# Kernel optimization log

Hardware: AMD Instinct MI355X
Metric: run time of the kernel (lower is better)

The kernel has to match this reference:

```python
import jax, jax.numpy as jnp
import numpy as np

N = 8192   # number of points
K = 16     # knn_graph k (loop=True -> self included)
C = 256    # conv hidden width
H = 128    # classifier hidden width


def _lin_init(key, fan_in, fan_out):
    s = 1.0 / np.sqrt(fan_in)
    kw, kb = jax.random.split(key)
    W = jax.random.uniform(kw, (fan_in, fan_out), minval=-s, maxval=s, dtype=jnp.float32)
    b = jax.random.uniform(kb, (fan_out,), minval=-s, maxval=s, dtype=jnp.float32)
    return W, b


def setup_inputs() -> dict:
    key = jax.random.key(0)
    ks = jax.random.split(key, 10)
    pos = jax.random.normal(ks[0], (N, 3), dtype=jnp.float32)
    # conv1 local_nn: Linear(3+3,256), ReLU, Linear(256,256)
    c1_W1, c1_b1 = _lin_init(ks[1], 3 + 3, C)
    c1_W2, c1_b2 = _lin_init(ks[2], C, C)
    # conv2/conv3 local_nn: Linear(256+3,256), ReLU, Linear(256,256)
    c2_W1, c2_b1 = _lin_init(ks[3], C + 3, C)
    c2_W2, c2_b2 = _lin_init(ks[4], C, C)
    c3_W1, c3_b1 = _lin_init(ks[5], C + 3, C)
    c3_W2, c3_b2 = _lin_init(ks[6], C, C)
    # classifier: Linear(256,128), ReLU, Linear(128,128), ReLU, Linear(128,1)
    h_W1, h_b1 = _lin_init(ks[7], C, H)
    h_W2, h_b2 = _lin_init(ks[8], H, H)
    h_W3, h_b3 = _lin_init(ks[9], H, 1)
    return dict(pos=pos,
                c1_W1=c1_W1, c1_b1=c1_b1, c1_W2=c1_W2, c1_b2=c1_b2,
                c2_W1=c2_W1, c2_b1=c2_b1, c2_W2=c2_W2, c2_b2=c2_b2,
                c3_W1=c3_W1, c3_b1=c3_b1, c3_W2=c3_W2, c3_b2=c3_b2,
                h_W1=h_W1, h_b1=h_b1, h_W2=h_W2, h_b2=h_b2, h_W3=h_W3, h_b3=h_b3)


def _knn_idx(pos):
    # squared pairwise distances via the gram trick; [N,N]
    sq = jnp.sum(pos * pos, axis=-1)
    d2 = sq[:, None] + sq[None, :] - 2.0 * (pos @ pos.T)
    # k smallest distances (self distance ~0 -> self loop, matching loop=True)
    _, idx = jax.lax.top_k(-d2, K)  # [N,K] neighbor (source) indices per target
    return idx


def _pointnet_conv(h, rel, idx, W1, b1, W2, b2):
    # message = local_nn(concat(x_j, pos_j - pos_i)); aggregate = max over neighbors
    e = jnp.concatenate([h[idx], rel], axis=-1)          # [N,K,Cin+3]
    m = jax.nn.relu(e @ W1 + b1) @ W2 + b2               # [N,K,C]
    return jnp.max(m, axis=1)                            # [N,C]


def reference(pos,
              c1_W1, c1_b1, c1_W2, c1_b2,
              c2_W1, c2_b1, c2_W2, c2_b2,
              c3_W1, c3_b1, c3_W2, c3_b2,
              h_W1, h_b1, h_W2, h_b2, h_W3, h_b3):
    idx = _knn_idx(pos)
    rel = pos[idx] - pos[:, None, :]                     # [N,K,3] relative coords
    h = pos                                              # train_with_norm=False
    h = jax.nn.relu(_pointnet_conv(h, rel, idx, c1_W1, c1_b1, c1_W2, c1_b2))
    h = jax.nn.relu(_pointnet_conv(h, rel, idx, c2_W1, c2_b1, c2_W2, c2_b2))
    h = jax.nn.relu(_pointnet_conv(h, rel, idx, c3_W1, c3_b1, c3_W2, c3_b2))
    h = jax.nn.relu(h @ h_W1 + h_b1)
    h = jax.nn.relu(h @ h_W2 + h_b2)
    return jax.nn.sigmoid(h @ h_W3 + h_b3)               # [N,1]
```

## Files before the change

### kernel.cpp

```cpp
#include <hip/hip_runtime.h>
#include <hip/hip_bf16.h>
#include <math.h>

#define NPTS 8192
#define CDIM 256
#define HDIM 128
#define NCH  32
#define CH   (NPTS / NCH)
#define CAP  48
#define NBKT 256

typedef __attribute__((ext_vector_type(8))) short bf16x8;
typedef __attribute__((ext_vector_type(4))) float f32x4;
typedef unsigned long long u64;

static __device__ __forceinline__ short f2bf(float f) {
  __hip_bfloat16 h = __float2bfloat16(f);
  return *reinterpret_cast<short*>(&h);
}

static __device__ __forceinline__ unsigned umed3(unsigned a, unsigned b,
                                                 unsigned c) {
  unsigned d;
  asm("v_med3_u32 %0, %1, %2, %3" : "=v"(d) : "v"(a), "v"(b), "v"(c));
  return d;
}

static __device__ __forceinline__ unsigned d2key(float4 p, float4 c) {
  float dot = fmaf(p.x, c.x, fmaf(p.y, c.y, p.z * c.z));
  float d2 = fmaf(-2.0f, dot, p.w + c.w);
  return __float_as_uint(fmaxf(d2, 0.0f));
}

static __device__ __forceinline__ int xbucket(float x) {
  int b = (int)floorf((x + 4.0f) * 32.0f);
  return min(max(b, 0), NBKT - 1);
}

#define U32INIT unsigned b0=~0u,b1=~0u,b2=~0u,b3=~0u,b4=~0u,b5=~0u,b6=~0u, \
                         b7=~0u,b8=~0u,b9=~0u,b10=~0u,b11=~0u,b12=~0u, \
                         b13=~0u,b14=~0u,b15=~0u;
#define U32CHAIN(key) { \
  b15 = umed3(b14, key, b15); b14 = umed3(b13, key, b14); \
  b13 = umed3(b12, key, b13); b12 = umed3(b11, key, b12); \
  b11 = umed3(b10, key, b11); b10 = umed3(b9,  key, b10); \
  b9  = umed3(b8,  key, b9);  b8  = umed3(b7,  key, b8);  \
  b7  = umed3(b6,  key, b7);  b6  = umed3(b5,  key, b6);  \
  b5  = umed3(b4,  key, b5);  b4  = umed3(b3,  key, b4);  \
  b3  = umed3(b2,  key, b3);  b2  = umed3(b1,  key, b2);  \
  b1  = umed3(b0,  key, b1);  b0  = min(b0, key); }

#define KSTEP(s) { bool sw_ = key < k##s; u64 t_ = k##s; \
                   k##s = sw_ ? key : t_; key = sw_ ? t_ : key; }
#define KCHAIN KSTEP(0) KSTEP(1) KSTEP(2) KSTEP(3) KSTEP(4) KSTEP(5) \
               KSTEP(6) KSTEP(7) KSTEP(8) KSTEP(9) KSTEP(10) KSTEP(11) \
               KSTEP(12) KSTEP(13) KSTEP(14) KSTEP(15)
#define KINIT u64 k0=~0ULL,k1=~0ULL,k2=~0ULL,k3=~0ULL,k4=~0ULL,k5=~0ULL, \
                  k6=~0ULL,k7=~0ULL,k8=~0ULL,k9=~0ULL,k10=~0ULL,k11=~0ULL, \
                  k12=~0ULL,k13=~0ULL,k14=~0ULL,k15=~0ULL;

__global__ __launch_bounds__(256) void prep_all(
    const float* __restrict__ c1W2, const float* __restrict__ c2W2,
    const float* __restrict__ c3W2, const float* __restrict__ c2W1,
    const float* __restrict__ c3W1, const float* __restrict__ hW1,
    const float* __restrict__ hW2,
    short* __restrict__ w2f1, short* __restrict__ w2f2,
    short* __restrict__ w2f3, short* __restrict__ wc2a,
    short* __restrict__ wc3a, short* __restrict__ whW1,
    short* __restrict__ whW2,
    unsigned* __restrict__ hist, unsigned* __restrict__ cursor) {
  int b = blockIdx.x, tid = threadIdx.x;
  if (b < 1280) {
    const float* W; short* wf; int rb;
    if (b < 256)       { W = c1W2; wf = w2f1; rb = b; }
    else if (b < 512)  { W = c2W2; wf = w2f2; rb = b - 256; }
    else if (b < 768)  { W = c3W2; wf = w2f3; rb = b - 512; }
    else if (b < 1024) { W = c2W1; wf = wc2a; rb = b - 768; }
    else               { W = c3W1; wf = wc3a; rb = b - 1024; }
    int t = rb * 256 + tid;
    int q = t & 7, l = (t >> 3) & 63, F = t >> 9;
    int ks = F & 7, c16 = F >> 3;
    int k = ks * 32 + ((l >> 4) << 3) + q;
    int c = c16 * 16 + (l & 15);
    wf[t] = f2bf(W[k * 256 + c]);
  } else if (b < 1408) {
    int t = (b - 1280) * 256 + tid;
    int q = t & 7, l = (t >> 3) & 63, F = t >> 9;
    int ks = F & 7, c16 = F >> 3;
    int k = ks * 32 + ((l >> 4) << 3) + q;
    int c = c16 * 16 + (l & 15);
    whW1[t] = f2bf(hW1[k * 128 + c]);
  } else if (b < 1472) {
    int t = (b - 1408) * 256 + tid;
    int q = t & 7, l = (t >> 3) & 63, F = t >> 9;
    int ks = F & 3, c16 = F >> 2;
    int k = ks * 32 + ((l >> 4) << 3) + q;
    int c = c16 * 16 + (l & 15);
    whW2[t] = f2bf(hW2[k * 128 + c]);
  } else {
    hist[tid] = 0u;
    cursor[tid] = 0u;
  }
}

__global__ __launch_bounds__(256) void hist_k(const float* __restrict__ pos,
                                              unsigned* __restrict__ hist) {
  int i = blockIdx.x * 256 + threadIdx.x;
  atomicAdd(&hist[xbucket(pos[3 * i])], 1u);
}

__global__ __launch_bounds__(256) void scan_k(const unsigned* __restrict__ hist,
                                              unsigned* __restrict__ base) {
  __shared__ unsigned s[NBKT];
  int t = threadIdx.x;
  unsigned h = hist[t];
  s[t] = h;
  __syncthreads();
  for (int off = 1; off < NBKT; off <<= 1) {
    unsigned v = (t >= off) ? s[t - off] : 0u;
    __syncthreads();
    s[t] += v;
    __syncthreads();
  }
  base[t] = s[t] - h;
}

__global__ __launch_bounds__(256) void scatter_k(
    const float* __restrict__ pos, const unsigned* __restrict__ base,
    unsigned* __restrict__ cursor, int* __restrict__ sidx,
    int* __restrict__ inv, float4* __restrict__ pos4) {
  int i = blockIdx.x * 256 + threadIdx.x;
  float x = pos[3 * i], y = pos[3 * i + 1], z = pos[3 * i + 2];
  int b = xbucket(x);
  unsigned slot = base[b] + atomicAdd(&cursor[b], 1u);
  sidx[slot] = i;
  inv[i] = (int)slot;
  pos4[slot] = make_float4(x, y, z, x * x + y * y + z * z);
}

__global__ __launch_bounds__(256) void knn_d2p1(const float4* __restrict__ pos4,
                                                unsigned* __restrict__ v) {
  __shared__ float4 cand[CH];
  __shared__ unsigned mbuf[128][16];
  int ch = blockIdx.x & (NCH - 1);
  int tgp = blockIdx.x >> 5;
  int tid = threadIdx.x;
  int i = tgp * 128 + (tid & 127);
  int half = tid >> 7;
  cand[tid] = pos4[ch * CH + tid];
  __syncthreads();

  float4 p = pos4[i];
  U32INIT
  int j0 = half * 128;
  for (int jj = 0; jj < 128; jj += 4) {
    float4 c0 = cand[j0 + jj],     c1 = cand[j0 + jj + 1];
    float4 c2 = cand[j0 + jj + 2], c3 = cand[j0 + jj + 3];
    unsigned x0 = d2key(p, c0), x1 = d2key(p, c1);
    unsigned x2 = d2key(p, c2), x3 = d2key(p, c3);
    U32CHAIN(x0) U32CHAIN(x1) U32CHAIN(x2) U32CHAIN(x3)
  }
  if (half) {
    unsigned* m = mbuf[tid - 128];
    m[0]=b0; m[1]=b1; m[2]=b2;  m[3]=b3;  m[4]=b4;  m[5]=b5;  m[6]=b6;  m[7]=b7;
    m[8]=b8; m[9]=b9; m[10]=b10;m[11]=b11;m[12]=b12;m[13]=b13;m[14]=b14;m[15]=b15;
  }
  __syncthreads();
  if (!half) {
#pragma unroll 1
    for (int s = 0; s < 16; ++s) {
      unsigned key = mbuf[tid][s];
      if (key >= b15) break;
      U32CHAIN(key)
    }
    uint4* dst = reinterpret_cast<uint4*>(v + ((size_t)ch * NPTS + i) * 16);
    dst[0] = make_uint4(b0, b1, b2, b3);
    dst[1] = make_uint4(b4, b5, b6, b7);
    dst[2] = make_uint4(b8, b9, b10, b11);
    dst[3] = make_uint4(b12, b13, b14, b15);
  }
}

__global__ __launch_bounds__(256) void knn_merge(const unsigned* __restrict__ v,
                                                 unsigned* __restrict__ T,
                                                 unsigned* __restrict__ cnt) {
  int wv = threadIdx.x >> 6, lane = threadIdx.x & 63;
  int i = blockIdx.x * 4 + wv;
  int ch = lane >> 1, half = lane & 1;
  const uint4* src = reinterpret_cast<const uint4*>(
      v + ((size_t)ch * NPTS + i) * 16 + half * 8);
  uint4 a = src[0], b = src[1];
  unsigned r1 = a.y, r2 = a.z, r3 = a.w;
  unsigned r4 = b.x, r5 = b.y, r6 = b.z, r7 = b.w;
  unsigned h = a.x;
  int idx = 0;
  unsigned wmin = 0;
#pragma unroll
  for (int round = 0; round < 16; ++round) {
    unsigned m = h;
    m = min(m, (unsigned)__shfl_xor((int)m, 1));
    m = min(m, (unsigned)__shfl_xor((int)m, 2));
    m = min(m, (unsigned)__shfl_xor((int)m, 4));
    m = min(m, (unsigned)__shfl_xor((int)m, 8));
    m = min(m, (unsigned)__shfl_xor((int)m, 16));
    m = min(m, (unsigned)__shfl_xor((int)m, 32));
    wmin = m;
    u64 ball = __ballot(h == m);
    int src_lane = __ffsll(ball) - 1;
    if (lane == src_lane) {
      ++idx;
      h = idx == 1 ? r1 : idx == 2 ? r2 : idx == 3 ? r3 : idx == 4 ? r4 :
          idx == 5 ? r5 : idx == 6 ? r6 : idx == 7 ? r7 : 0xFFFFFFFFu;
    }
  }
  if (lane == 0) { T[i] = wmin; cnt[i] = 0; }
}

__global__ __launch_bounds__(256) void knn_d2p2(const float4* __restrict__ pos4,
                                                const int* __restrict__ sidx,
                                                const unsigned* __restrict__ T,
                                                unsigned* __restrict__ cnt,
                                                u64* __restrict__ cbuf) {
  __shared__ float4 cand[CH];
  __shared__ int sj[CH];
  int ch = blockIdx.x & (NCH - 1);
  int tgp = blockIdx.x >> 5;
  int tid = threadIdx.x;
  int i = tgp * 128 + (tid & 127);
  int half = tid >> 7;
  cand[tid] = pos4[ch * CH + tid];
  sj[tid] = sidx[ch * CH + tid];
  __syncthreads();

  float4 p = pos4[i];
  unsigned Ti = T[i];
  int j0 = half * 128;
  for (int jj = 0; jj < 128; jj += 8) {
    unsigned k[8];
#pragma unroll
    for (int u = 0; u < 8; ++u) k[u] = d2key(p, cand[j0 + jj + u]);
    unsigned m = min(min(min(k[0], k[1]), min(k[2], k[3])),
                     min(min(k[4], k[5]), min(k[6], k[7])));
    if (m <= Ti) {
#pragma unroll
      for (int u = 0; u < 8; ++u) {
        if (k[u] <= Ti) {
          unsigned slot = atomicAdd(&cnt[i], 1u);
          if (slot < CAP)
            cbuf[(size_t)i * CAP + slot] =
                ((u64)k[u] << 32) | (unsigned)sj[j0 + jj + u];
        }
      }
    }
  }
}

__global__ __launch_bounds__(256) void knn_select(const unsigned* __restrict__ cnt,
                                                  const u64* __restrict__ cbuf,
                                                  const int* __restrict__ inv,
                                                  int* __restrict__ idx_out) {
  int i = blockIdx.x * 256 + threadIdx.x;
  int c = (int)min(cnt[i], (unsigned)CAP);
  KINIT
#pragma unroll 1
  for (int q = 0; q < c; ++q) {
    u64 key = cbuf[(size_t)i * CAP + q];
    if (key < k15) { KCHAIN }
  }
  int* o = idx_out + i * 16;
  o[0]=inv[(unsigned)k0];   o[1]=inv[(unsigned)k1];   o[2]=inv[(unsigned)k2];
  o[3]=inv[(unsigned)k3];   o[4]=inv[(unsigned)k4];   o[5]=inv[(unsigned)k5];
  o[6]=inv[(unsigned)k6];   o[7]=inv[(unsigned)k7];   o[8]=inv[(unsigned)k8];
  o[9]=inv[(unsigned)k9];   o[10]=inv[(unsigned)k10]; o[11]=inv[(unsigned)k11];
  o[12]=inv[(unsigned)k12]; o[13]=inv[(unsigned)k13]; o[14]=inv[(unsigned)k14];
  o[15]=inv[(unsigned)k15];
}

__global__ __launch_bounds__(256) void tu1_prep(const float4* __restrict__ pos4,
                                                const float* __restrict__ W1,
                                                const float* __restrict__ b1,
                                                float* __restrict__ TU) {
  int c = threadIdx.x;
  float w0 = W1[c]       + W1[768 + c];
  float w1 = W1[256 + c] + W1[1024 + c];
  float w2 = W1[512 + c] + W1[1280 + c];
  float bv = b1[c];
#pragma unroll
  for (int r = 0; r < 4; ++r) {
    int i = blockIdx.x * 4 + r;
    float4 P = pos4[i];
    TU[(size_t)i * 256 + c] = fmaf(P.x, w0, fmaf(P.y, w1, fmaf(P.z, w2, bv)));
  }
}

template <int NCOLS, int KDIM, int ACT, int ADDP>
__global__ __launch_bounds__(256) void gemm_mfma(
    const float* __restrict__ A,
    const short* __restrict__ wf,
    const float* __restrict__ bias,
    const float4* __restrict__ pos4,
    const float* __restrict__ W1p,
    float* __restrict__ out) {
  constexpr int KS = KDIM / 32;
  constexpr int NF = NCOLS / 64;
  __shared__ __align__(16) short As[32 * KDIM];

  int tid = threadIdx.x;
  int row0 = blockIdx.x * 32;

  {
    int row = tid & 31, wq = tid >> 5;
    const float* Ar = A + (size_t)(row0 + row) * KDIM;
#pragma unroll
    for (int q = 0; q < KDIM / 64; ++q) {
      int c0 = wq * 8 + q * 64;
      float4 a = *reinterpret_cast<const float4*>(Ar + c0);
      float4 b = *reinterpret_cast<const float4*>(Ar + c0 + 4);
      bf16x8 o;
      o[0] = f2bf(a.x); o[1] = f2bf(a.y); o[2] = f2bf(a.z); o[3] = f2bf(a.w);
      o[4] = f2bf(b.x); o[5] = f2bf(b.y); o[6] = f2bf(b.z); o[7] = f2bf(b.w);
      int byte = row * (KDIM * 2) + c0 * 2;
      byte ^= (row & 7) << 4;
      *reinterpret_cast<bf16x8*>(reinterpret_cast<char*>(As) + byte) = o;
    }
  }
  __syncthreads();

  int l = tid & 63, w = tid >> 6;
  int lhi = l >> 4, llo = l & 15;
  f32x4 zero = {0.f, 0.f, 0.f, 0.f};
  f32x4 acc[2][NF];
#pragma unroll
  for (int m = 0; m < 2; ++m)
#pragma unroll
    for (int n = 0; n < NF; ++n) acc[m][n] = zero;

  const bf16x8* WfV = reinterpret_cast<const bf16x8*>(wf);
#pragma unroll
  for (int ks = 0; ks < KS; ++ks) {
    bf16x8 af[2], bfr[NF];
#pragma unroll
    for (int m = 0; m < 2; ++m) {
      int r = m * 16 + llo;
      int byte = r * (KDIM * 2) + ks * 64 + lhi * 16;
      byte ^= (r & 7) << 4;
      af[m] = *reinterpret_cast<const bf16x8*>(
          reinterpret_cast<const char*>(As) + byte);
    }
#pragma unroll
    for (int n = 0; n < NF; ++n)
      bfr[n] = WfV[((w * NF + n) * KS + ks) * 64 + l];
#pragma unroll
    for (int m = 0; m < 2; ++m)
#pragma unroll
      for (int n = 0; n < NF; ++n)
        acc[m][n] = __builtin_amdgcn_mfma_f32_16x16x32_bf16(af[m], bfr[n],
                                                            acc[m][n], 0, 0, 0);
  }

  int cc[NF];
  float bv[NF], u0[NF], u1[NF], u2[NF];
#pragma unroll
  for (int n = 0; n < NF; ++n) {
    cc[n] = (w * NF + n) * 16 + llo;
    bv[n] = bias[cc[n]];
    if constexpr (ADDP) {
      u0[n] = W1p[cc[n]];
      u1[n] = W1p[NCOLS + cc[n]];
      u2[n] = W1p[2 * NCOLS + cc[n]];
    } else { u0[n] = u1[n] = u2[n] = 0.f; }
  }
#pragma unroll
  for (int m = 0; m < 2; ++m)
#pragma unroll
    for (int j = 0; j < 4; ++j) {
      int r = row0 + m * 16 + lhi * 4 + j;
      float px = 0.f, py = 0.f, pz = 0.f;
      if constexpr (ADDP) {
        float4 P = pos4[r];
        px = P.x; py = P.y; pz = P.z;
      }
#pragma unroll
      for (int n = 0; n < NF; ++n) {
        float v = acc[m][n][j] + bv[n];
        if constexpr (ADDP) v += px * u0[n] + py * u1[n] + pz * u2[n];
        if (ACT == 1) v = fmaxf(v, 0.0f);
        out[(size_t)r * NCOLS + cc[n]] = v;
      }
    }
}

__global__ __launch_bounds__(256) void conv_mfma(
    const float* __restrict__ TU,
    const float4* __restrict__ pos4,
    const int* __restrict__ idx,
    const float* __restrict__ W1p,
    const short* __restrict__ w2f,
    const float* __restrict__ b2,
    float* __restrict__ hout) {
  __shared__ __align__(16) short m1s[64 * 256];
  __shared__ float Ub[4][256];
  __shared__ int js[64];

  int tid = threadIdx.x;
  int t0 = blockIdx.x * 4;
  if (tid < 64) js[tid] = idx[(t0 + (tid >> 4)) * 16 + (tid & 15)];
#pragma unroll
  for (int q = 0; q < 4; ++q) {
    int e = tid + 256 * q;
    int tg = e >> 8, c = e & 255;
    float4 P = pos4[t0 + tg];
    Ub[tg][c] = P.x * W1p[c] + P.y * W1p[256 + c] + P.z * W1p[512 + c];
  }
  __syncthreads();

  {
    int row = tid & 63;
    int wq = tid >> 6;
    int jrow = js[row];
    const float* TUj = TU + (size_t)jrow * 256;
    const float* Ui = &Ub[row >> 4][0];
#pragma unroll
    for (int q = 0; q < 8; ++q) {
      int c0 = wq * 8 + q * 32;
      float4 a = *reinterpret_cast<const float4*>(TUj + c0);
      float4 b = *reinterpret_cast<const float4*>(TUj + c0 + 4);
      float4 ua = *reinterpret_cast<const float4*>(Ui + c0);
      float4 ub = *reinterpret_cast<const float4*>(Ui + c0 + 4);
      bf16x8 o;
      o[0] = f2bf(fmaxf(a.x - ua.x, 0.f));
      o[1] = f2bf(fmaxf(a.y - ua.y, 0.f));
      o[2] = f2bf(fmaxf(a.z - ua.z, 0.f));
      o[3] = f2bf(fmaxf(a.w - ua.w, 0.f));
      o[4] = f2bf(fmaxf(b.x - ub.x, 0.f));
      o[5] = f2bf(fmaxf(b.y - ub.y, 0.f));
      o[6] = f2bf(fmaxf(b.z - ub.z, 0.f));
      o[7] = f2bf(fmaxf(b.w - ub.w, 0.f));
      int byte = row * 512 + c0 * 2;
      byte ^= (row & 7) << 4;
      *reinterpret_cast<bf16x8*>(reinterpret_cast<char*>(m1s) + byte) = o;
    }
  }
  __syncthreads();

  int l = tid & 63, w = tid >> 6;
  int lhi = l >> 4, llo = l & 15;
  f32x4 zero = {0.f, 0.f, 0.f, 0.f};
  f32x4 acc[4][4];
#pragma unroll
  for (int m = 0; m < 4; ++m)
#pragma unroll
    for (int n = 0; n < 4; ++n) acc[m][n] = zero;

  const bf16x8* Wf = reinterpret_cast<const bf16x8*>(w2f);
#pragma unroll
  for (int ks = 0; ks < 8; ++ks) {
    int k0 = ks * 32;
    bf16x8 af[4], bfr[4];
#pragma unroll
    for (int m = 0; m < 4; ++m) {
      int r = m * 16 + llo;
      int byte = r * 512 + k0 * 2 + lhi * 16;
      byte ^= (r & 7) << 4;
      af[m] = *reinterpret_cast<const bf16x8*>(
          reinterpret_cast<const char*>(m1s) + byte);
    }
#pragma unroll
    for (int n = 0; n < 4; ++n)
      bfr[n] = Wf[((w * 4 + n) * 8 + ks) * 64 + l];
#pragma unroll
    for (int m = 0; m < 4; ++m)
#pragma unroll
      for (int n = 0; n < 4; ++n)
        acc[m][n] = __builtin_amdgcn_mfma_f32_16x16x32_bf16(af[m], bfr[n],
                                                            acc[m][n], 0, 0, 0);
  }

#pragma unroll
  for (int m = 0; m < 4; ++m)
#pragma unroll
    for (int n = 0; n < 4; ++n) {
      float v = fmaxf(fmaxf(acc[m][n][0], acc[m][n][1]),
                      fmaxf(acc[m][n][2], acc[m][n][3]));
      v = fmaxf(v, __shfl_xor(v, 16));
      v = fmaxf(v, __shfl_xor(v, 32));
      if (lhi == 0) {
        int c = w * 64 + n * 16 + llo;
        hout[(size_t)(t0 + m) * CDIM + c] = fmaxf(v + b2[c], 0.0f);
      }
    }
}

__global__ __launch_bounds__(64) void final_k(const float* __restrict__ h2,
                                              const float* __restrict__ w3,
                                              const float* __restrict__ b3,
                                              const int* __restrict__ sidx,
                                              float* __restrict__ out) {
  int r = blockIdx.x, l = threadIdx.x;
  float s = h2[(size_t)r * HDIM + l] * w3[l] +
            h2[(size_t)r * HDIM + 64 + l] * w3[64 + l];
#pragma unroll
  for (int o = 32; o > 0; o >>= 1) s += __shfl_down(s, o);
  if (l == 0) out[sidx[r]] = 1.0f / (1.0f + expf(-(s + b3[0])));
}

extern "C" void kernel_launch(void* const* d_in, const int* in_sizes, int n_in,
                              void* d_out, int out_size, void* d_ws,
                              size_t ws_size, hipStream_t stream) {
  const float* pos   = (const float*)d_in[0];
  const float* c1_W1 = (const float*)d_in[1];
  const float* c1_b1 = (const float*)d_in[2];
  const float* c1_W2 = (const float*)d_in[3];
  const float* c1_b2 = (const float*)d_in[4];
  const float* c2_W1 = (const float*)d_in[5];
  const float* c2_b1 = (const float*)d_in[6];
  const float* c2_W2 = (const float*)d_in[7];
  const float* c2_b2 = (const float*)d_in[8];
  const float* c3_W1 = (const float*)d_in[9];
  const float* c3_b1 = (const float*)d_in[10];
  const float* c3_W2 = (const float*)d_in[11];
  const float* c3_b2 = (const float*)d_in[12];
  const float* h_W1  = (const float*)d_in[13];
  const float* h_b1  = (const float*)d_in[14];
  const float* h_W2  = (const float*)d_in[15];
  const float* h_b2  = (const float*)d_in[16];
  const float* h_W3  = (const float*)d_in[17];
  const float* h_b3  = (const float*)d_in[18];
  float* out = (float*)d_out;

  char* w = (char*)d_ws;
  const size_t MB = 1 << 20;
  const size_t KB = 1 << 10;
  int*      p_idx  = (int*)w;
  float4*   p_pos4 = (float4*)(w + 512 * KB);
  unsigned* p_T    = (unsigned*)(w + 640 * KB);
  unsigned* p_cnt  = (unsigned*)(w + 672 * KB);
  short*    p_w2f1 = (short*)(w + 704 * KB);
  short*    p_w2f2 = (short*)(w + 832 * KB);
  short*    p_w2f3 = (short*)(w + 960 * KB);
  short*    p_wc2a = (short*)(w + 1088 * KB);
  short*    p_wc3a = (short*)(w + 1216 * KB);
  short*    p_whW1 = (short*)(w + 1344 * KB);
  short*    p_whW2 = (short*)(w + 1408 * KB);
  unsigned* p_hist = (unsigned*)(w + 1440 * KB);
  unsigned* p_base = (unsigned*)(w + 1441 * KB);
  unsigned* p_cur  = (unsigned*)(w + 1442 * KB);
  int*      p_sidx = (int*)(w + 1444 * KB);
  int*      p_inv  = (int*)(w + 1476 * KB);
  u64*      p_cbuf = (u64*)(w + 1536 * KB);
  float*    p_TU   = (float*)(w + 5 * MB);
  unsigned* p_v    = (unsigned*)(w + 13 * MB);
  float*    p_hA   = (float*)(w + 13 * MB);
  float*    p_hB   = (float*)(w + 21 * MB);
  float*    p_c1   = (float*)(w + 5 * MB);
  float*    p_c2   = (float*)(w + 9 * MB);

  prep_all<<<1473, 256, 0, stream>>>(
      c1_W2, c2_W2, c3_W2, c2_W1, c3_W1, h_W1, h_W2,
      p_w2f1, p_w2f2, p_w2f3, p_wc2a, p_wc3a, p_whW1, p_whW2, p_hist, p_cur);

  hist_k<<<NPTS / 256, 256, 0, stream>>>(pos, p_hist);
  scan_k<<<1, 256, 0, stream>>>(p_hist, p_base);
  scatter_k<<<NPTS / 256, 256, 0, stream>>>(pos, p_base, p_cur,
                                            p_sidx, p_inv, p_pos4);

  tu1_prep<<<NPTS / 4, 256, 0, stream>>>(p_pos4, c1_W1, c1_b1, p_TU);

  knn_d2p1<<<(NPTS / 128) * NCH, 256, 0, stream>>>(p_pos4, p_v);
  knn_merge<<<NPTS / 4, 256, 0, stream>>>(p_v, p_T, p_cnt);
  knn_d2p2<<<(NPTS / 128) * NCH, 256, 0, stream>>>(p_pos4, p_sidx, p_T,
                                                   p_cnt, p_cbuf);
  knn_select<<<NPTS / 256, 256, 0, stream>>>(p_cnt, p_cbuf, p_inv, p_idx);

  conv_mfma<<<NPTS / 4, 256, 0, stream>>>(p_TU, p_pos4, p_idx, c1_W1 + 3 * 256,
                                          p_w2f1, c1_b2, p_hA);
  gemm_mfma<256, 256, 0, 1><<<NPTS / 32, 256, 0, stream>>>(
      p_hA, p_wc2a, c2_b1, p_pos4, c2_W1 + 256 * 256, p_TU);
  conv_mfma<<<NPTS / 4, 256, 0, stream>>>(p_TU, p_pos4, p_idx,
                                          c2_W1 + 256 * 256, p_w2f2, c2_b2, p_hB);
  gemm_mfma<256, 256, 0, 1><<<NPTS / 32, 256, 0, stream>>>(
      p_hB, p_wc3a, c3_b1, p_pos4, c3_W1 + 256 * 256, p_TU);
  conv_mfma<<<NPTS / 4, 256, 0, stream>>>(p_TU, p_pos4, p_idx,
                                          c3_W1 + 256 * 256, p_w2f3, c3_b2, p_hA);
  gemm_mfma<128, 256, 1, 0><<<NPTS / 32, 256, 0, stream>>>(
      p_hA, p_whW1, h_b1, nullptr, nullptr, p_c1);
  gemm_mfma<128, 128, 1, 0><<<NPTS / 32, 256, 0, stream>>>(
      p_c1, p_whW2, h_b2, nullptr, nullptr, p_c2);
  final_k<<<NPTS, 64, 0, stream>>>(p_c2, h_W3, h_b3, p_sidx, out);

  (void)in_sizes; (void)n_in; (void)out_size; (void)ws_size;
}
```

Measured before the change: 308.9 us.

## Prune KNN chunk-target block pairs using x-range bounds and radius estimates

Adds a knn_own pass that computes, for each 128-point target group, the largest 16th-neighbour distance within its own chunk, plus x-coordinate bounds for chunks and target groups. knn_d2p1, knn_merge and knn_d2p2 then skip chunk/target pairs whose x-gap squared exceeds that radius, since points are sorted by x bucket. The aim is to avoid most of the all-pairs distance work in both passes. The cost is an extra kernel launch and some reductions, and correctness now relies on the bound, which is padded by a small relative margin.

```diff
diff --git a/kernel.cpp b/kernel.cpp
--- a/kernel.cpp
+++ b/kernel.cpp
@@ -35,6 +35,12 @@
 static __device__ __forceinline__ int xbucket(float x) {
   int b = (int)floorf((x + 4.0f) * 32.0f);
   return min(max(b, 0), NBKT - 1);
+}
+
+static __device__ __forceinline__ bool win_hit(float clo, float chi,
+                                               float tlo, float thi, float R) {
+  float g = fmaxf(fmaxf(clo - thi, tlo - chi), 0.0f);
+  return g * g <= R;
 }
 
 #define U32INIT unsigned b0=~0u,b1=~0u,b2=~0u,b3=~0u,b4=~0u,b5=~0u,b6=~0u, \
@@ -110,9 +116,11 @@
 }
 
 __global__ __launch_bounds__(256) void scan_k(const unsigned* __restrict__ hist,
-                                              unsigned* __restrict__ base) {
+                                              unsigned* __restrict__ base,
+                                              unsigned* __restrict__ tmax) {
   __shared__ unsigned s[NBKT];
   int t = threadIdx.x;
+  if (t < 64) tmax[t] = 0u;
   unsigned h = hist[t];
   s[t] = h;
   __syncthreads();
@@ -138,12 +146,90 @@
   pos4[slot] = make_float4(x, y, z, x * x + y * y + z * z);
 }
 
-__global__ __launch_bounds__(256) void knn_d2p1(const float4* __restrict__ pos4,
-                                                unsigned* __restrict__ v) {
+__global__ __launch_bounds__(256) void knn_own(const float4* __restrict__ pos4,
+                                               float* __restrict__ Umax,
+                                               float* __restrict__ chbnd,
+                                               float* __restrict__ tb) {
   __shared__ float4 cand[CH];
   __shared__ unsigned mbuf[128][16];
+  __shared__ float rmin[256], rmax[256];
+  int ch = blockIdx.x >> 1, th = blockIdx.x & 1;
+  int tid = threadIdx.x;
+  cand[tid] = pos4[ch * CH + tid];
+  __syncthreads();
+
+  int t = tid & 127, half = tid >> 7;
+  float4 p = cand[th * 128 + t];
+  U32INIT
+  int j0 = half * 128;
+  for (int jj = 0; jj < 128; jj += 4) {
+    float4 c0 = cand[j0 + jj],     c1 = cand[j0 + jj + 1];
+    float4 c2 = cand[j0 + jj + 2], c3 = cand[j0 + jj + 3];
+    unsigned x0 = d2key(p, c0), x1 = d2key(p, c1);
+    unsigned x2 = d2key(p, c2), x3 = d2key(p, c3);
+    U32CHAIN(x0) U32CHAIN(x1) U32CHAIN(x2) U32CHAIN(x3)
+  }
+  if (half) {
+    unsigned* m = mbuf[t];
+    m[0]=b0; m[1]=b1; m[2]=b2;  m[3]=b3;  m[4]=b4;  m[5]=b5;  m[6]=b6;  m[7]=b7;
+    m[8]=b8; m[9]=b9; m[10]=b10;m[11]=b11;m[12]=b12;m[13]=b13;m[14]=b14;m[15]=b15;
+  }
+  __syncthreads();
+  float Ui = 0.0f;
+  if (!half) {
+#pragma unroll 1
+    for (int s = 0; s < 16; ++s) {
+      unsigned key = mbuf[t][s];
+      if (key >= b15) break;
+      U32CHAIN(key)
+    }
+    Ui = __uint_as_float(b15);
+  }
+  rmin[tid] = cand[tid].x; rmax[tid] = cand[tid].x;
+  __syncthreads();
+  for (int off = 128; off; off >>= 1) {
+    if (tid < off) {
+      rmin[tid] = fminf(rmin[tid], rmin[tid + off]);
+      rmax[tid] = fmaxf(rmax[tid], rmax[tid + off]);
+    }
+    __syncthreads();
+  }
+  if (tid == 0) { chbnd[2 * ch] = rmin[0]; chbnd[2 * ch + 1] = rmax[0]; }
+  __syncthreads();
+  rmin[tid] = cand[th * 128 + t].x; rmax[tid] = rmin[tid];
+  __syncthreads();
+  for (int off = 128; off; off >>= 1) {
+    if (tid < off) {
+      rmin[tid] = fminf(rmin[tid], rmin[tid + off]);
+      rmax[tid] = fmaxf(rmax[tid], rmax[tid + off]);
+    }
+    __syncthreads();
+  }
+  int tgp = ch * 2 + th;
+  if (tid == 0) { tb[2 * tgp] = rmin[0]; tb[2 * tgp + 1] = rmax[0]; }
+  __syncthreads();
+  rmax[tid] = (!half) ? Ui : 0.0f;
+  __syncthreads();
+  for (int off = 128; off; off >>= 1) {
+    if (tid < off) rmax[tid] = fmaxf(rmax[tid], rmax[tid + off]);
+    __syncthreads();
+  }
+  if (tid == 0) Umax[tgp] = rmax[0];
+}
+
+__global__ __launch_bounds__(256) void knn_d2p1(const float4* __restrict__ pos4,
+                                                const float* __restrict__ Umax,
+                                                const float* __restrict__ chbnd,
+                                                const float* __restrict__ tb,
+                                                unsigned* __restrict__ v) {
   int ch = blockIdx.x & (NCH - 1);
   int tgp = blockIdx.x >> 5;
+  float R = Umax[tgp] * 1.0001f;
+  if (!win_hit(chbnd[2 * ch], chbnd[2 * ch + 1],
+               tb[2 * tgp], tb[2 * tgp + 1], R)) return;
+
+  __shared__ float4 cand[CH];
+  __shared__ unsigned mbuf[128][16];
   int tid = threadIdx.x;
   int i = tgp * 128 + (tid & 127);
   int half = tid >> 7;
@@ -182,17 +268,28 @@
 }
 
 __global__ __launch_bounds__(256) void knn_merge(const unsigned* __restrict__ v,
+                                                 const float* __restrict__ Umax,
+                                                 const float* __restrict__ chbnd,
+                                                 const float* __restrict__ tb,
                                                  unsigned* __restrict__ T,
-                                                 unsigned* __restrict__ cnt) {
+                                                 unsigned* __restrict__ cnt,
+                                                 unsigned* __restrict__ tmax) {
   int wv = threadIdx.x >> 6, lane = threadIdx.x & 63;
   int i = blockIdx.x * 4 + wv;
   int ch = lane >> 1, half = lane & 1;
-  const uint4* src = reinterpret_cast<const uint4*>(
-      v + ((size_t)ch * NPTS + i) * 16 + half * 8);
-  uint4 a = src[0], b = src[1];
-  unsigned r1 = a.y, r2 = a.z, r3 = a.w;
-  unsigned r4 = b.x, r5 = b.y, r6 = b.z, r7 = b.w;
-  unsigned h = a.x;
+  int tgp = i >> 7;
+  float R = Umax[tgp] * 1.0001f;
+  bool hit = win_hit(chbnd[2 * ch], chbnd[2 * ch + 1],
+                     tb[2 * tgp], tb[2 * tgp + 1], R);
+  unsigned h = ~0u, r1 = ~0u, r2 = ~0u, r3 = ~0u,
+           r4 = ~0u, r5 = ~0u, r6 = ~0u, r7 = ~0u;
+  if (hit) {
+    const uint4* src = reinterpret_cast<const uint4*>(
+        v + ((size_t)ch * NPTS + i) * 16 + half * 8);
+    uint4 a = src[0], b = src[1];
+    h = a.x; r1 = a.y; r2 = a.z; r3 = a.w;
+    r4 = b.x; r5 = b.y; r6 = b.z; r7 = b.w;
+  }
   int idx = 0;
   unsigned wmin = 0;
 #pragma unroll
@@ -213,18 +310,29 @@
           idx == 5 ? r5 : idx == 6 ? r6 : idx == 7 ? r7 : 0xFFFFFFFFu;
     }
   }
-  if (lane == 0) { T[i] = wmin; cnt[i] = 0; }
+  if (lane == 0) {
+    T[i] = wmin;
+    cnt[i] = 0;
+    atomicMax(&tmax[tgp], wmin);
+  }
 }
 
 __global__ __launch_bounds__(256) void knn_d2p2(const float4* __restrict__ pos4,
                                                 const int* __restrict__ sidx,
                                                 const unsigned* __restrict__ T,
+                                                const unsigned* __restrict__ tmax,
+                                                const float* __restrict__ chbnd,
+                                                const float* __restrict__ tb,
                                                 unsigned* __restrict__ cnt,
                                                 u64* __restrict__ cbuf) {
+  int ch = blockIdx.x & (NCH - 1);
+  int tgp = blockIdx.x >> 5;
+  float R = __uint_as_float(tmax[tgp]) * 1.0001f;
+  if (!win_hit(chbnd[2 * ch], chbnd[2 * ch + 1],
+               tb[2 * tgp], tb[2 * tgp + 1], R)) return;
+
   __shared__ float4 cand[CH];
   __shared__ int sj[CH];
-  int ch = blockIdx.x & (NCH - 1);
-  int tgp = blockIdx.x >> 5;
   int tid = threadIdx.x;
   int i = tgp * 128 + (tid & 127);
   int half = tid >> 7;
@@ -548,6 +656,10 @@
   int*      p_sidx = (int*)(w + 1444 * KB);
   int*      p_inv  = (int*)(w + 1476 * KB);
   u64*      p_cbuf = (u64*)(w + 1536 * KB);
+  float*    p_umax = (float*)(w + 4608 * KB);
+  float*    p_chb  = (float*)(w + 4609 * KB);
+  float*    p_tb   = (float*)(w + 4610 * KB);
+  unsigned* p_tmax = (unsigned*)(w + 4612 * KB);
   float*    p_TU   = (float*)(w + 5 * MB);
   unsigned* p_v    = (unsigned*)(w + 13 * MB);
   float*    p_hA   = (float*)(w + 13 * MB);
@@ -560,16 +672,19 @@
       p_w2f1, p_w2f2, p_w2f3, p_wc2a, p_wc3a, p_whW1, p_whW2, p_hist, p_cur);
 
   hist_k<<<NPTS / 256, 256, 0, stream>>>(pos, p_hist);
-  scan_k<<<1, 256, 0, stream>>>(p_hist, p_base);
+  scan_k<<<1, 256, 0, stream>>>(p_hist, p_base, p_tmax);
   scatter_k<<<NPTS / 256, 256, 0, stream>>>(pos, p_base, p_cur,
                                             p_sidx, p_inv, p_pos4);
 
   tu1_prep<<<NPTS / 4, 256, 0, stream>>>(p_pos4, c1_W1, c1_b1, p_TU);
 
-  knn_d2p1<<<(NPTS / 128) * NCH, 256, 0, stream>>>(p_pos4, p_v);
-  knn_merge<<<NPTS / 4, 256, 0, stream>>>(p_v, p_T, p_cnt);
-  knn_d2p2<<<(NPTS / 128) * NCH, 256, 0, stream>>>(p_pos4, p_sidx, p_T,
-                                                   p_cnt, p_cbuf);
+  knn_own<<<NCH * 2, 256, 0, stream>>>(p_pos4, p_umax, p_chb, p_tb);
+  knn_d2p1<<<(NPTS / 128) * NCH, 256, 0, stream>>>(p_pos4, p_umax, p_chb,
+                                                   p_tb, p_v);
+  knn_merge<<<NPTS / 4, 256, 0, stream>>>(p_v, p_umax, p_chb, p_tb,
+                                          p_T, p_cnt, p_tmax);
+  knn_d2p2<<<(NPTS / 128) * NCH, 256, 0, stream>>>(p_pos4, p_sidx, p_T, p_tmax,
+                                                   p_chb, p_tb, p_cnt, p_cbuf);
   knn_select<<<NPTS / 256, 256, 0, stream>>>(p_cnt, p_cbuf, p_inv, p_idx);
 
   conv_mfma<<<NPTS / 4, 256, 0, stream>>>(p_TU, p_pos4, p_idx, c1_W1 + 3 * 256,
```

Result: slower. 372.6 us (+20.6%).

## Fuse kNN into one kernel with x-sorted chunk pruning

Applied to the files above, without the earlier changes.

Replaces the four-kernel brute-force kNN (per-chunk top-16, global merge, threshold replay, select) with one fused kernel. Each block handles 32 targets, with 8 threads per target. It scans its own x-sorted chunk and then expands left and right, stopping once a chunk's x-gap squared exceeds the block's current worst 16th distance. Candidates are replayed into shared-memory queues, and the final top-16 is merged by shuffles. This is meant to skip most distance evaluations and the global-memory intermediates, but it serialises chunk scanning with many barriers and launches fewer blocks.

```diff
diff --git a/kernel.cpp b/kernel.cpp
--- a/kernel.cpp
+++ b/kernel.cpp
@@ -7,7 +7,7 @@
 #define HDIM 128
 #define NCH  32
 #define CH   (NPTS / NCH)
-#define CAP  48
+#define QCAP 48
 #define NBKT 256
 
 typedef __attribute__((ext_vector_type(8))) short bf16x8;
@@ -35,6 +35,13 @@
 static __device__ __forceinline__ int xbucket(float x) {
   int b = (int)floorf((x + 4.0f) * 32.0f);
   return min(max(b, 0), NBKT - 1);
+}
+
+static __device__ __forceinline__ u64 shfl_xor_u64(u64 v, int m) {
+  unsigned lo = (unsigned)v, hi = (unsigned)(v >> 32);
+  lo = (unsigned)__shfl_xor((int)lo, m);
+  hi = (unsigned)__shfl_xor((int)hi, m);
+  return ((u64)hi << 32) | lo;
 }
 
 #define U32INIT unsigned b0=~0u,b1=~0u,b2=~0u,b3=~0u,b4=~0u,b5=~0u,b6=~0u, \
@@ -138,142 +145,165 @@
   pos4[slot] = make_float4(x, y, z, x * x + y * y + z * z);
 }
 
-__global__ __launch_bounds__(256) void knn_d2p1(const float4* __restrict__ pos4,
-                                                unsigned* __restrict__ v) {
+__global__ __launch_bounds__(256) void chbnd_k(const float4* __restrict__ pos4,
+                                               float* __restrict__ chbnd) {
+  __shared__ float rmin[256], rmax[256];
+  int ch = blockIdx.x, tid = threadIdx.x;
+  float x = pos4[ch * CH + tid].x;
+  rmin[tid] = x; rmax[tid] = x;
+  __syncthreads();
+  for (int off = 128; off; off >>= 1) {
+    if (tid < off) {
+      rmin[tid] = fminf(rmin[tid], rmin[tid + off]);
+      rmax[tid] = fmaxf(rmax[tid], rmax[tid + off]);
+    }
+    __syncthreads();
+  }
+  if (tid == 0) { chbnd[2 * ch] = rmin[0]; chbnd[2 * ch + 1] = rmax[0]; }
+}
+
+#define SCAN_CHUNK(chv) { \
+    cand[tid] = pos4[(size_t)(chv) * CH + tid]; \
+    __syncthreads(); \
+    int j0_ = sl * 32; \
+    for (int jj_ = 0; jj_ < 32; jj_ += 4) { \
+      float4 c0_ = cand[j0_ + jj_],     c1_ = cand[j0_ + jj_ + 1]; \
+      float4 c2_ = cand[j0_ + jj_ + 2], c3_ = cand[j0_ + jj_ + 3]; \
+      unsigned x0_ = d2key(p, c0_), x1_ = d2key(p, c1_); \
+      unsigned x2_ = d2key(p, c2_), x3_ = d2key(p, c3_); \
+      U32CHAIN(x0_) U32CHAIN(x1_) U32CHAIN(x2_) U32CHAIN(x3_) \
+    } \
+    __syncthreads(); }
+
+#define BLOCK_MAXB15(outv) { \
+    red[tid] = b15; __syncthreads(); \
+    for (int off_ = 128; off_; off_ >>= 1) { \
+      if (tid < off_) red[tid] = max(red[tid], red[tid + off_]); \
+      __syncthreads(); } \
+    outv = red[0]; __syncthreads(); }
+
+#define REPLAY_CHUNK(chv) { \
+    cand[tid] = pos4[(size_t)(chv) * CH + tid]; \
+    sj[tid] = sidx[(size_t)(chv) * CH + tid]; \
+    __syncthreads(); \
+    for (int jj_ = 0; jj_ < 32; ++jj_) { \
+      int c_ = sl * 32 + jj_; \
+      unsigned key_ = d2key(p, cand[c_]); \
+      if (key_ <= T) { \
+        unsigned pos_ = atomicAdd(&qcnt[tl], 1u); \
+        if (pos_ < QCAP) qbuf[tl][pos_] = ((u64)key_ << 32) | (unsigned)sj[c_]; \
+      } \
+    } \
+    __syncthreads(); }
+
+__global__ __launch_bounds__(256) void knn_fused(
+    const float4* __restrict__ pos4, const int* __restrict__ sidx,
+    const int* __restrict__ inv, const float* __restrict__ chbnd,
+    int* __restrict__ idx_out) {
   __shared__ float4 cand[CH];
-  __shared__ unsigned mbuf[128][16];
-  int ch = blockIdx.x & (NCH - 1);
-  int tgp = blockIdx.x >> 5;
+  __shared__ int sj[CH];
+  __shared__ unsigned red[256];
+  __shared__ u64 qbuf[32][QCAP];
+  __shared__ unsigned qcnt[32];
+  __shared__ float fred[32];
+  __shared__ float gb[2];
+
   int tid = threadIdx.x;
-  int i = tgp * 128 + (tid & 127);
-  int half = tid >> 7;
-  cand[tid] = pos4[ch * CH + tid];
-  __syncthreads();
-
+  int tl = tid >> 3, sl = tid & 7;
+  int i = blockIdx.x * 32 + tl;
+  int own = blockIdx.x >> 3;
   float4 p = pos4[i];
+  int lane = tid & 63;
+  int gbase = lane & ~7;
+
+  if (tid < 32) fred[tid] = pos4[blockIdx.x * 32 + tid].x;
+  __syncthreads();
+  if (tid == 0) {
+    float lo = fred[0], hi = fred[0];
+    for (int q = 1; q < 32; ++q) { lo = fminf(lo, fred[q]); hi = fmaxf(hi, fred[q]); }
+    gb[0] = lo; gb[1] = hi;
+  }
+  __syncthreads();
+  float tlo = gb[0], thi = gb[1];
+
   U32INIT
-  int j0 = half * 128;
-  for (int jj = 0; jj < 128; jj += 4) {
-    float4 c0 = cand[j0 + jj],     c1 = cand[j0 + jj + 1];
-    float4 c2 = cand[j0 + jj + 2], c3 = cand[j0 + jj + 3];
-    unsigned x0 = d2key(p, c0), x1 = d2key(p, c1);
-    unsigned x2 = d2key(p, c2), x3 = d2key(p, c3);
-    U32CHAIN(x0) U32CHAIN(x1) U32CHAIN(x2) U32CHAIN(x3)
-  }
-  if (half) {
-    unsigned* m = mbuf[tid - 128];
-    m[0]=b0; m[1]=b1; m[2]=b2;  m[3]=b3;  m[4]=b4;  m[5]=b5;  m[6]=b6;  m[7]=b7;
-    m[8]=b8; m[9]=b9; m[10]=b10;m[11]=b11;m[12]=b12;m[13]=b13;m[14]=b14;m[15]=b15;
-  }
-  __syncthreads();
-  if (!half) {
-#pragma unroll 1
-    for (int s = 0; s < 16; ++s) {
-      unsigned key = mbuf[tid][s];
-      if (key >= b15) break;
-      U32CHAIN(key)
-    }
-    uint4* dst = reinterpret_cast<uint4*>(v + ((size_t)ch * NPTS + i) * 16);
-    dst[0] = make_uint4(b0, b1, b2, b3);
-    dst[1] = make_uint4(b4, b5, b6, b7);
-    dst[2] = make_uint4(b8, b9, b10, b11);
-    dst[3] = make_uint4(b12, b13, b14, b15);
-  }
-}
-
-__global__ __launch_bounds__(256) void knn_merge(const unsigned* __restrict__ v,
-                                                 unsigned* __restrict__ T,
-                                                 unsigned* __restrict__ cnt) {
-  int wv = threadIdx.x >> 6, lane = threadIdx.x & 63;
-  int i = blockIdx.x * 4 + wv;
-  int ch = lane >> 1, half = lane & 1;
-  const uint4* src = reinterpret_cast<const uint4*>(
-      v + ((size_t)ch * NPTS + i) * 16 + half * 8);
-  uint4 a = src[0], b = src[1];
-  unsigned r1 = a.y, r2 = a.z, r3 = a.w;
-  unsigned r4 = b.x, r5 = b.y, r6 = b.z, r7 = b.w;
-  unsigned h = a.x;
-  int idx = 0;
-  unsigned wmin = 0;
-#pragma unroll
-  for (int round = 0; round < 16; ++round) {
+  SCAN_CHUNK(own)
+  int nl = 0, nr = 0;
+  bool doneL = (own == 0), doneR = (own == NCH - 1);
+  while (!doneL || !doneR) {
+    unsigned bound;
+    BLOCK_MAXB15(bound)
+    float B = __uint_as_float(bound) * 1.0001f;
+    if (!doneL) {
+      int ch = own - 1 - nl;
+      float g = tlo - chbnd[2 * ch + 1];
+      if (g > 0.0f && g * g > B) doneL = true;
+      else { SCAN_CHUNK(ch) ++nl; doneL = (own - 1 - nl < 0); }
+    }
+    if (!doneR) {
+      int ch = own + 1 + nr;
+      float g = chbnd[2 * ch] - thi;
+      if (g > 0.0f && g * g > B) doneR = true;
+      else { SCAN_CHUNK(ch) ++nr; doneR = (own + 1 + nr >= NCH); }
+    }
+  }
+
+  unsigned h = b0;
+  unsigned T = 0;
+#pragma unroll
+  for (int r = 0; r < 16; ++r) {
     unsigned m = h;
     m = min(m, (unsigned)__shfl_xor((int)m, 1));
     m = min(m, (unsigned)__shfl_xor((int)m, 2));
     m = min(m, (unsigned)__shfl_xor((int)m, 4));
-    m = min(m, (unsigned)__shfl_xor((int)m, 8));
-    m = min(m, (unsigned)__shfl_xor((int)m, 16));
-    m = min(m, (unsigned)__shfl_xor((int)m, 32));
-    wmin = m;
     u64 ball = __ballot(h == m);
-    int src_lane = __ffsll(ball) - 1;
-    if (lane == src_lane) {
-      ++idx;
-      h = idx == 1 ? r1 : idx == 2 ? r2 : idx == 3 ? r3 : idx == 4 ? r4 :
-          idx == 5 ? r5 : idx == 6 ? r6 : idx == 7 ? r7 : 0xFFFFFFFFu;
-    }
-  }
-  if (lane == 0) { T[i] = wmin; cnt[i] = 0; }
-}
-
-__global__ __launch_bounds__(256) void knn_d2p2(const float4* __restrict__ pos4,
-                                                const int* __restrict__ sidx,
-                                                const unsigned* __restrict__ T,
-                                                unsigned* __restrict__ cnt,
-                                                u64* __restrict__ cbuf) {
-  __shared__ float4 cand[CH];
-  __shared__ int sj[CH];
-  int ch = blockIdx.x & (NCH - 1);
-  int tgp = blockIdx.x >> 5;
-  int tid = threadIdx.x;
-  int i = tgp * 128 + (tid & 127);
-  int half = tid >> 7;
-  cand[tid] = pos4[ch * CH + tid];
-  sj[tid] = sidx[ch * CH + tid];
-  __syncthreads();
-
-  float4 p = pos4[i];
-  unsigned Ti = T[i];
-  int j0 = half * 128;
-  for (int jj = 0; jj < 128; jj += 8) {
-    unsigned k[8];
-#pragma unroll
-    for (int u = 0; u < 8; ++u) k[u] = d2key(p, cand[j0 + jj + u]);
-    unsigned m = min(min(min(k[0], k[1]), min(k[2], k[3])),
-                     min(min(k[4], k[5]), min(k[6], k[7])));
-    if (m <= Ti) {
-#pragma unroll
-      for (int u = 0; u < 8; ++u) {
-        if (k[u] <= Ti) {
-          unsigned slot = atomicAdd(&cnt[i], 1u);
-          if (slot < CAP)
-            cbuf[(size_t)i * CAP + slot] =
-                ((u64)k[u] << 32) | (unsigned)sj[j0 + jj + u];
-        }
-      }
-    }
-  }
-}
-
-__global__ __launch_bounds__(256) void knn_select(const unsigned* __restrict__ cnt,
-                                                  const u64* __restrict__ cbuf,
-                                                  const int* __restrict__ inv,
-                                                  int* __restrict__ idx_out) {
-  int i = blockIdx.x * 256 + threadIdx.x;
-  int c = (int)min(cnt[i], (unsigned)CAP);
+    unsigned gball = (unsigned)((ball >> gbase) & 0xFFull);
+    bool adv = ((lane - gbase) == (__ffs((int)gball) - 1));
+    h   = adv ? b1  : h;   b1  = adv ? b2  : b1;
+    b2  = adv ? b3  : b2;  b3  = adv ? b4  : b3;
+    b4  = adv ? b5  : b4;  b5  = adv ? b6  : b5;
+    b6  = adv ? b7  : b6;  b7  = adv ? b8  : b7;
+    b8  = adv ? b9  : b8;  b9  = adv ? b10 : b9;
+    b10 = adv ? b11 : b10; b11 = adv ? b12 : b11;
+    b12 = adv ? b13 : b12; b13 = adv ? b14 : b13;
+    b14 = adv ? b15 : b14; b15 = adv ? 0xFFFFFFFFu : b15;
+    T = m;
+  }
+
+  if (tid < 32) qcnt[tid] = 0;
+  __syncthreads();
+  REPLAY_CHUNK(own)
+  for (int q = 0; q < nl; ++q) REPLAY_CHUNK(own - 1 - q)
+  for (int q = 0; q < nr; ++q) REPLAY_CHUNK(own + 1 + q)
+
+  int n = (int)min(qcnt[tl], (unsigned)QCAP);
   KINIT
-#pragma unroll 1
-  for (int q = 0; q < c; ++q) {
-    u64 key = cbuf[(size_t)i * CAP + q];
+  for (int q = sl; q < n; q += 8) {
+    u64 key = qbuf[tl][q];
     if (key < k15) { KCHAIN }
   }
-  int* o = idx_out + i * 16;
-  o[0]=inv[(unsigned)k0];   o[1]=inv[(unsigned)k1];   o[2]=inv[(unsigned)k2];
-  o[3]=inv[(unsigned)k3];   o[4]=inv[(unsigned)k4];   o[5]=inv[(unsigned)k5];
-  o[6]=inv[(unsigned)k6];   o[7]=inv[(unsigned)k7];   o[8]=inv[(unsigned)k8];
-  o[9]=inv[(unsigned)k9];   o[10]=inv[(unsigned)k10]; o[11]=inv[(unsigned)k11];
-  o[12]=inv[(unsigned)k12]; o[13]=inv[(unsigned)k13]; o[14]=inv[(unsigned)k14];
-  o[15]=inv[(unsigned)k15];
+  u64 hh = k0;
+  int* o = idx_out + (size_t)i * 16;
+#pragma unroll
+  for (int r = 0; r < 16; ++r) {
+    u64 m = hh;
+    u64 s_;
+    s_ = shfl_xor_u64(m, 1); m = s_ < m ? s_ : m;
+    s_ = shfl_xor_u64(m, 2); m = s_ < m ? s_ : m;
+    s_ = shfl_xor_u64(m, 4); m = s_ < m ? s_ : m;
+    u64 ball = __ballot(hh == m);
+    unsigned gball = (unsigned)((ball >> gbase) & 0xFFull);
+    bool adv = ((lane - gbase) == (__ffs((int)gball) - 1));
+    hh  = adv ? k1  : hh;  k1  = adv ? k2  : k1;
+    k2  = adv ? k3  : k2;  k3  = adv ? k4  : k3;
+    k4  = adv ? k5  : k4;  k5  = adv ? k6  : k5;
+    k6  = adv ? k7  : k6;  k7  = adv ? k8  : k7;
+    k8  = adv ? k9  : k8;  k9  = adv ? k10 : k9;
+    k10 = adv ? k11 : k10; k11 = adv ? k12 : k11;
+    k12 = adv ? k13 : k12; k13 = adv ? k14 : k13;
+    k14 = adv ? k15 : k14; k15 = adv ? ~0ULL : k15;
+    if (sl == 0) o[r] = inv[(unsigned)m];
+  }
 }
 
 __global__ __launch_bounds__(256) void tu1_prep(const float4* __restrict__ pos4,
@@ -533,8 +563,6 @@
   const size_t KB = 1 << 10;
   int*      p_idx  = (int*)w;
   float4*   p_pos4 = (float4*)(w + 512 * KB);
-  unsigned* p_T    = (unsigned*)(w + 640 * KB);
-  unsigned* p_cnt  = (unsigned*)(w + 672 * KB);
   short*    p_w2f1 = (short*)(w + 704 * KB);
   short*    p_w2f2 = (short*)(w + 832 * KB);
   short*    p_w2f3 = (short*)(w + 960 * KB);
@@ -547,9 +575,8 @@
   unsigned* p_cur  = (unsigned*)(w + 1442 * KB);
   int*      p_sidx = (int*)(w + 1444 * KB);
   int*      p_inv  = (int*)(w + 1476 * KB);
-  u64*      p_cbuf = (u64*)(w + 1536 * KB);
+  float*    p_chb  = (float*)(w + 1508 * KB);
   float*    p_TU   = (float*)(w + 5 * MB);
-  unsigned* p_v    = (unsigned*)(w + 13 * MB);
   float*    p_hA   = (float*)(w + 13 * MB);
   float*    p_hB   = (float*)(w + 21 * MB);
   float*    p_c1   = (float*)(w + 5 * MB);
@@ -566,11 +593,8 @@
 
   tu1_prep<<<NPTS / 4, 256, 0, stream>>>(p_pos4, c1_W1, c1_b1, p_TU);
 
-  knn_d2p1<<<(NPTS / 128) * NCH, 256, 0, stream>>>(p_pos4, p_v);
-  knn_merge<<<NPTS / 4, 256, 0, stream>>>(p_v, p_T, p_cnt);
-  knn_d2p2<<<(NPTS / 128) * NCH, 256, 0, stream>>>(p_pos4, p_sidx, p_T,
-                                                   p_cnt, p_cbuf);
-  knn_select<<<NPTS / 256, 256, 0, stream>>>(p_cnt, p_cbuf, p_inv, p_idx);
+  chbnd_k<<<NCH, 256, 0, stream>>>(p_pos4, p_chb);
+  knn_fused<<<NPTS / 32, 256, 0, stream>>>(p_pos4, p_sidx, p_inv, p_chb, p_idx);
 
   conv_mfma<<<NPTS / 4, 256, 0, stream>>>(p_TU, p_pos4, p_idx, c1_W1 + 3 * 256,
                                           p_w2f1, c1_b2, p_hA);
```

After: 375.5 us. 1.22x slower.
